# Kernel tuning notes

Hardware: AMD Instinct MI355X
Metric: run time of the kernel (lower is better)

The kernel has to match this reference:

```python
import jax, jax.numpy as jnp
jax.config.update("jax_enable_x64", True)
import numpy as np

B_, H_, W_, O_ = 8, 96, 96, 8
STRIDES = 1


def generate_px_coordinates(shape, coord_K, strides=1):
    # coord_K: [B,2,2]; row 0 = per-axis scale, row 1 = per-axis offset
    H, W = shape
    u = jnp.arange(W, dtype=coord_K.dtype)[None, None, :]
    v = jnp.arange(H, dtype=coord_K.dtype)[None, :, None]
    u = u * strides * coord_K[:, 0, 0][:, None, None] + coord_K[:, 1, 0][:, None, None]
    v = v * strides * coord_K[:, 0, 1][:, None, None] + coord_K[:, 1, 1][:, None, None]
    B = coord_K.shape[0]
    return jnp.broadcast_to(u, (B, H, W)), jnp.broadcast_to(v, (B, H, W))


def matrix_A(obj, TCR):
    # obj: [B,H,W,O,3]; TCR: [B,4,4] -> A: [B,H,W,O,4,13]
    p1 = obj[..., 0:1]
    p2 = obj[..., 1:2]
    p3 = obj[..., 2:3]
    one = jnp.ones_like(p1)
    T1 = TCR[:, None, None, None, :, 0]
    T2 = TCR[:, None, None, None, :, 1]
    T3 = TCR[:, None, None, None, :, 2]
    T4 = TCR[:, None, None, None, :, 3]
    return jnp.stack((p1 * T1, p2 * T1, p3 * T1,
                      p1 * T2, p2 * T2, p3 * T2,
                      p1 * T3, p2 * T3, p3 * T3,
                      one * T4, one * T1, one * T2, one * T3), axis=-1)


def matrix_B(shape, camera_matrix, coord_K, strides=1):
    # -> [B,H,W,2,4]
    u, v = generate_px_coordinates(shape, coord_K, strides)
    coords = jnp.stack([u, v], axis=-1)[..., None]  # [B,H,W,2,1]
    left4 = -jnp.eye(2, dtype=camera_matrix.dtype)[None, None, None] \
            * camera_matrix[:, None, None, :2, :2]  # [B,H,W,2,2]
    Bn, H, W = u.shape
    left4 = jnp.broadcast_to(left4, (Bn, H, W, 2, 2))
    d1_2 = coords - camera_matrix[:, None, None, :2, 2:3]  # [B,H,W,2,1]
    return jnp.concatenate([left4, d1_2, jnp.zeros_like(d1_2)], axis=-1)


def setup_inputs() -> dict:
    key = jax.random.key(0)
    k1, k2, k3, k4 = jax.random.split(key, 4)
    obj = jax.random.normal(k1, (B_, H_, W_, O_, 3), dtype=jnp.float32)
    w_pixel = jax.random.normal(k2, (B_, H_, W_, O_, 4), dtype=jnp.float32)
    camera_matrix = jax.random.normal(k3, (B_, 3, 3), dtype=jnp.float32)
    coord_K = jax.random.uniform(k4, (B_, 2, 2), dtype=jnp.float32)
    return {"obj": obj, "w_pixel": w_pixel,
            "camera_matrix": camera_matrix, "coord_K": coord_K}


def reference(obj, w_pixel, camera_matrix, coord_K):
    B, H, W, O = obj.shape[:4]
    Wp = w_pixel.reshape(B, H, W, O, 2, 2)
    TCR = jnp.broadcast_to(jnp.eye(4, dtype=obj.dtype), (B, 4, 4))
    A = matrix_A(obj, TCR)                                  # [B,H,W,O,4,13]
    Bm = matrix_B((H, W), camera_matrix, coord_K, STRIDES)  # [B,H,W,2,4]
    BA = jnp.einsum('bxyij,bxyojk->bxyoik', Bm, A)          # [B,H,W,O,2,13]
    MRow = jnp.matmul(Wp, BA)                               # [B,H,W,O,2,13]
    num_eq = 2 * H * W
    M = jnp.transpose(MRow, (0, 3, 1, 2, 4, 5)).reshape(B, O, num_eq, 13)
    M = M.astype(jnp.float64)
    return jnp.matmul(jnp.swapaxes(M, -1, -2), M)           # [B,O,13,13]
```

## Files before the change

kernel.cpp:

```cpp
#include <hip/hip_runtime.h>

#define B_ 8
#define H_ 96
#define W_ 96
#define O_ 8
#define HW_ (H_ * W_)
#define NT 512
#define NCH 72
#define PPB (HW_ / NCH)
#define ITERS (PPB / 64)

__global__ __launch_bounds__(NT) void mtm_partial(
    const float* __restrict__ obj,
    const float* __restrict__ wpx,
    const float* __restrict__ cam,
    const float* __restrict__ ck,
    float* __restrict__ ws)
{
    const int chunk = blockIdx.x;
    const int b     = blockIdx.y;

    const float* cm = cam + b * 9;
    const float* k4 = ck  + b * 4;
    const float a   = -cm[0];
    const float c   = -cm[4];
    const float k00 = k4[0];
    const float k01 = k4[1];
    const float Bu  = k4[2] - cm[2];
    const float Bv  = k4[3] - cm[5];

    const int o  = threadIdx.x & 7;
    const int pg = threadIdx.x >> 3;

    float acc[60];
#pragma unroll
    for (int s = 0; s < 60; ++s) acc[s] = 0.f;

#pragma unroll
    for (int it = 0; it < ITERS; ++it) {
        const int p = chunk * PPB + it * 64 + pg;
        const int h = p / W_;
        const int w = p - h * W_;
        const int slot = (b * HW_ + p) * O_ + o;

        const float* ob = obj + (size_t)slot * 3;
        const float p1 = ob[0], p2 = ob[1], p3 = ob[2];
        const float4 wp = *(const float4*)(wpx + (size_t)slot * 4);

        const float du = fmaf((float)w, k00, Bu);
        const float dv = fmaf((float)h, k01, Bv);

        const float x00 = wp.x * a;
        const float x01 = wp.y * c;
        const float x02 = fmaf(wp.x, du, wp.y * dv);
        const float x10 = wp.z * a;
        const float x11 = wp.w * c;
        const float x12 = fmaf(wp.z, du, wp.w * dv);

        float Xa[6];
        Xa[0] = fmaf(x00, x00, x10 * x10);
        Xa[1] = fmaf(x00, x01, x10 * x11);
        Xa[2] = fmaf(x00, x02, x10 * x12);
        Xa[3] = fmaf(x01, x01, x11 * x11);
        Xa[4] = fmaf(x01, x02, x11 * x12);
        Xa[5] = fmaf(x02, x02, x12 * x12);

        float Q[10];
        Q[0] = p1 * p1; Q[1] = p1 * p2; Q[2] = p1 * p3; Q[3] = p1;
        Q[4] = p2 * p2; Q[5] = p2 * p3; Q[6] = p2;
        Q[7] = p3 * p3; Q[8] = p3;
        Q[9] = 1.f;

#pragma unroll
        for (int ij = 0; ij < 6; ++ij) {
#pragma unroll
            for (int kl = 0; kl < 10; ++kl)
                acc[ij * 10 + kl] = fmaf(Xa[ij], Q[kl], acc[ij * 10 + kl]);
        }
    }

#pragma unroll
    for (int s = 0; s < 60; ++s) {
        float v = acc[s];
        v += __shfl_xor(v, 8,  64);
        v += __shfl_xor(v, 16, 64);
        v += __shfl_xor(v, 32, 64);
        acc[s] = v;
    }

    __shared__ float lds[64 * 60];
    const int lane = threadIdx.x & 63;
    const int wave = threadIdx.x >> 6;
    if (lane < 8) {
#pragma unroll
        for (int s = 0; s < 60; ++s)
            lds[(wave * 8 + lane) * 60 + s] = acc[s];
    }
    __syncthreads();

    if (threadIdx.x < 480) {
        const int oo = threadIdx.x / 60;
        const int ss = threadIdx.x - oo * 60;
        float v = 0.f;
#pragma unroll
        for (int w = 0; w < 8; ++w) v += lds[(w * 8 + oo) * 60 + ss];
        ws[((size_t)b * NCH + chunk) * 480 + threadIdx.x] = v;
    }
}

__global__ __launch_bounds__(256) void mtm_reduce(
    const float* __restrict__ ws,
    float* __restrict__ out)
{
    const int bo = blockIdx.x;
    const int b  = bo >> 3;
    const int o  = bo & 7;
    const int t  = threadIdx.x;

    __shared__ float S4[60][4];
    __shared__ float S[60];

    if (t < 240) {
        const int s = t >> 2, part = t & 3;
        float v = 0.f;
#pragma unroll
        for (int ch = part; ch < NCH; ch += 4)
            v += ws[((size_t)b * NCH + ch) * 480 + o * 60 + s];
        S4[s][part] = v;
    }
    __syncthreads();
    if (t < 60) S[t] = S4[t][0] + S4[t][1] + S4[t][2] + S4[t][3];
    __syncthreads();

    if (t < 169) {
        const int r  = t / 13;
        const int cc = t - r * 13;
        float val = 0.f;
        if (r != 9 && cc != 9) {
            int i, k, j, l;
            if (r < 9)  { i = r / 3;  k = r - i * 3; } else { i = r - 10;  k = 3; }
            if (cc < 9) { j = cc / 3; l = cc - j * 3; } else { j = cc - 10; l = 3; }
            const int ii = i < j ? i : j, jj = i < j ? j : i;
            const int kk = k < l ? k : l, ll = k < l ? l : k;
            const int ijIdx = ii * (5 - ii) / 2 + jj;
            const int klIdx = kk * (7 - kk) / 2 + ll;
            val = S[ijIdx * 10 + klIdx];
        }
        out[(size_t)bo * 169 + t] = val;
    }
}

extern "C" void kernel_launch(void* const* d_in, const int* in_sizes, int n_in,
                              void* d_out, int out_size, void* d_ws, size_t ws_size,
                              hipStream_t stream) {
    const float* obj = (const float*)d_in[0];
    const float* wpx = (const float*)d_in[1];
    const float* cam = (const float*)d_in[2];
    const float* ck  = (const float*)d_in[3];
    float* ws  = (float*)d_ws;
    float* out = (float*)d_out;

    mtm_partial<<<dim3(NCH, B_), dim3(NT), 0, stream>>>(obj, wpx, cam, ck, ws);
    mtm_reduce<<<dim3(B_ * O_), dim3(256), 0, stream>>>(ws, out);
}
```

Baseline: 87.37 us.

## Fuse partial and reduce kernels into one cooperative kernel with grid sync

Merges the two-kernel partial-sum and reduction pipeline into a single cooperative launch that uses a grid-wide barrier before the final reduction. Block size and chunk count change (256 threads, 32 chunks per batch), so each thread processes more pixels and the grid has 256 blocks. This removes a kernel launch and the gap between launches, but adds grid-sync overhead and cooperative-launch constraints. Parallelism also drops from 576 blocks of 512 threads to 256 blocks of 256 threads, which may underfill the GPU.

```diff
diff --git a/kernel.cpp b/kernel.cpp
--- a/kernel.cpp
+++ b/kernel.cpp
@@ -1,24 +1,31 @@
 #include <hip/hip_runtime.h>
+#include <hip/hip_cooperative_groups.h>
+
+namespace cg = cooperative_groups;
 
 #define B_ 8
 #define H_ 96
 #define W_ 96
 #define O_ 8
 #define HW_ (H_ * W_)
-#define NT 512
-#define NCH 72
+#define NT 256
+#define NCH 32
 #define PPB (HW_ / NCH)
-#define ITERS (PPB / 64)
+#define PG (NT / O_)
+#define ITERS (PPB / PG)
+#define NBLK (B_ * NCH)
 
-__global__ __launch_bounds__(NT) void mtm_partial(
+__global__ __launch_bounds__(NT) void mtm_coop(
     const float* __restrict__ obj,
     const float* __restrict__ wpx,
     const float* __restrict__ cam,
     const float* __restrict__ ck,
-    float* __restrict__ ws)
+    float* __restrict__ ws,
+    float* __restrict__ out)
 {
-    const int chunk = blockIdx.x;
-    const int b     = blockIdx.y;
+    const int bid   = blockIdx.x;
+    const int b     = bid >> 5;
+    const int chunk = bid & (NCH - 1);
 
     const float* cm = cam + b * 9;
     const float* k4 = ck  + b * 4;
@@ -38,7 +45,7 @@
 
 #pragma unroll
     for (int it = 0; it < ITERS; ++it) {
-        const int p = chunk * PPB + it * 64 + pg;
+        const int p = chunk * PPB + it * PG + pg;
         const int h = p / W_;
         const int w = p - h * W_;
         const int slot = (b * HW_ + p) * O_ + o;
@@ -88,7 +95,7 @@
         acc[s] = v;
     }
 
-    __shared__ float lds[64 * 60];
+    __shared__ float lds[4 * 8 * 60];
     const int lane = threadIdx.x & 63;
     const int wave = threadIdx.x >> 6;
     if (lane < 8) {
@@ -98,55 +105,54 @@
     }
     __syncthreads();
 
-    if (threadIdx.x < 480) {
-        const int oo = threadIdx.x / 60;
-        const int ss = threadIdx.x - oo * 60;
+    for (int idx = threadIdx.x; idx < 480; idx += NT) {
+        const int oo = idx / 60;
+        const int ss = idx - oo * 60;
         float v = 0.f;
 #pragma unroll
-        for (int w = 0; w < 8; ++w) v += lds[(w * 8 + oo) * 60 + ss];
-        ws[((size_t)b * NCH + chunk) * 480 + threadIdx.x] = v;
+        for (int w = 0; w < 4; ++w) v += lds[(w * 8 + oo) * 60 + ss];
+        ws[(size_t)bid * 480 + idx] = v;
     }
-}
 
-__global__ __launch_bounds__(256) void mtm_reduce(
-    const float* __restrict__ ws,
-    float* __restrict__ out)
-{
-    const int bo = blockIdx.x;
-    const int b  = bo >> 3;
-    const int o  = bo & 7;
-    const int t  = threadIdx.x;
+    cg::this_grid().sync();
 
-    __shared__ float S4[60][4];
-    __shared__ float S[60];
+    if (bid < B_ * O_) {
+        const int b2 = bid >> 3;
+        const int o2 = bid & 7;
+        const int t  = threadIdx.x;
 
-    if (t < 240) {
-        const int s = t >> 2, part = t & 3;
-        float v = 0.f;
+        float* S4 = lds;
+        float* S  = lds + 240;
+
+        if (t < 240) {
+            const int s = t >> 2, part = t & 3;
+            float v = 0.f;
 #pragma unroll
-        for (int ch = part; ch < NCH; ch += 4)
-            v += ws[((size_t)b * NCH + ch) * 480 + o * 60 + s];
-        S4[s][part] = v;
-    }
-    __syncthreads();
-    if (t < 60) S[t] = S4[t][0] + S4[t][1] + S4[t][2] + S4[t][3];
-    __syncthreads();
+            for (int ch = part; ch < NCH; ch += 4)
+                v += ws[((size_t)(b2 * NCH + ch)) * 480 + o2 * 60 + s];
+            S4[s * 4 + part] = v;
+        }
+        __syncthreads();
+        if (t < 60)
+            S[t] = S4[t * 4] + S4[t * 4 + 1] + S4[t * 4 + 2] + S4[t * 4 + 3];
+        __syncthreads();
 
-    if (t < 169) {
-        const int r  = t / 13;
-        const int cc = t - r * 13;
-        float val = 0.f;
-        if (r != 9 && cc != 9) {
-            int i, k, j, l;
-            if (r < 9)  { i = r / 3;  k = r - i * 3; } else { i = r - 10;  k = 3; }
-            if (cc < 9) { j = cc / 3; l = cc - j * 3; } else { j = cc - 10; l = 3; }
-            const int ii = i < j ? i : j, jj = i < j ? j : i;
-            const int kk = k < l ? k : l, ll = k < l ? l : k;
-            const int ijIdx = ii * (5 - ii) / 2 + jj;
-            const int klIdx = kk * (7 - kk) / 2 + ll;
-            val = S[ijIdx * 10 + klIdx];
+        if (t < 169) {
+            const int r  = t / 13;
+            const int cc = t - r * 13;
+            float val = 0.f;
+            if (r != 9 && cc != 9) {
+                int i, k, j, l;
+                if (r < 9)  { i = r / 3;  k = r - i * 3; } else { i = r - 10;  k = 3; }
+                if (cc < 9) { j = cc / 3; l = cc - j * 3; } else { j = cc - 10; l = 3; }
+                const int ii = i < j ? i : j, jj = i < j ? j : i;
+                const int kk = k < l ? k : l, ll = k < l ? l : k;
+                const int ijIdx = ii * (5 - ii) / 2 + jj;
+                const int klIdx = kk * (7 - kk) / 2 + ll;
+                val = S[ijIdx * 10 + klIdx];
+            }
+            out[(size_t)bid * 169 + t] = val;
         }
-        out[(size_t)bo * 169 + t] = val;
     }
 }
 
@@ -160,6 +166,8 @@
     float* ws  = (float*)d_ws;
     float* out = (float*)d_out;
 
-    mtm_partial<<<dim3(NCH, B_), dim3(NT), 0, stream>>>(obj, wpx, cam, ck, ws);
-    mtm_reduce<<<dim3(B_ * O_), dim3(256), 0, stream>>>(ws, out);
+    void* args[] = {(void*)&obj, (void*)&wpx, (void*)&cam, (void*)&ck,
+                    (void*)&ws, (void*)&out};
+    hipLaunchCooperativeKernel((const void*)mtm_coop, dim3(NBLK), dim3(NT),
+                               args, 0, stream);
 }
```

After: 110.7 us. 26.7% more time.
